# Kernel optimization log

Measured on AMD Instinct MI355X. Metric: run time of the kernel, lower is better.

The kernel has to match this reference:

```python
import jax, jax.numpy as jnp
import numpy as np

WS = 7
NUM_HEADS = 4


def setup_inputs() -> dict:
    key = jax.random.key(0)
    ks = jax.random.split(key, 5)
    C = 128
    return {
        "x": jax.random.normal(ks[0], (8, 222, 222, C), dtype=jnp.float32),
        "qkv_w": jax.random.normal(ks[1], (C, 3 * C), dtype=jnp.float32) * 0.02,
        "qkv_b": jax.random.normal(ks[2], (3 * C,), dtype=jnp.float32) * 0.02,
        "proj_w": jax.random.normal(ks[3], (C, C), dtype=jnp.float32) * 0.02,
        "proj_b": jax.random.normal(ks[4], (C,), dtype=jnp.float32) * 0.02,
    }


def reference(x, qkv_w, qkv_b, proj_w, proj_b):
    B, H, W, C = x.shape
    ws, nh = WS, NUM_HEADS
    hd = C // nh
    scale = hd ** (-0.5)
    pad_h = (ws - H % ws) % ws
    pad_w = (ws - W % ws) % ws
    xp = jnp.pad(x, ((0, 0), (0, pad_h), (0, pad_w), (0, 0)))
    Hp, Wp = H + pad_h, W + pad_w
    # window partition: [B,Hp,Wp,C] -> [nW, ws*ws, C]
    xw = xp.reshape(B, Hp // ws, ws, Wp // ws, ws, C)
    xw = xw.transpose(0, 1, 3, 2, 4, 5).reshape(-1, ws * ws, C)
    # qkv projection
    qkv = xw @ qkv_w + qkv_b  # [nW, 49, 3C]
    qkv = qkv.reshape(-1, ws * ws, 3, nh, hd).transpose(2, 0, 3, 1, 4)
    q, k, v = qkv[0], qkv[1], qkv[2]  # each [nW, nh, 49, hd]
    attn = jax.nn.softmax(jnp.einsum('whqd,whkd->whqk', q, k) * scale, axis=-1)
    out = jnp.einsum('whqk,whkd->whqd', attn, v)  # [nW, nh, 49, hd]
    out = out.transpose(0, 2, 1, 3).reshape(-1, ws * ws, C)
    out = out @ proj_w + proj_b
    # window reverse: [nW, ws*ws, C] -> [B, Hp, Wp, C]
    out = out.reshape(B, Hp // ws, Wp // ws, ws, ws, C)
    out = out.transpose(0, 1, 3, 2, 4, 5).reshape(B, Hp, Wp, C)
    return out[:, :H, :W, :]
```

## Files before the change

kernel.cpp:

```cpp
#include <hip/hip_runtime.h>
#include <stdint.h>

typedef __attribute__((ext_vector_type(8))) short bf16x8;
typedef __attribute__((ext_vector_type(4))) float f32x4;

#define IMG 222

__device__ __forceinline__ unsigned short f2bf(float f){
  unsigned int u = __float_as_uint(f);
  return (unsigned short)((u + 0x7fffu + ((u >> 16) & 1u)) >> 16);
}

__device__ __forceinline__ int sw128(int r, int c){ return r*128 + (c ^ ((r & 7) << 3)); }
__device__ __forceinline__ int sw64 (int r, int c){ return r*64  + (c ^ ((r & 7) << 3)); }

__global__ void prep_weights(const float* __restrict__ qkv_w,
                             const float* __restrict__ proj_w,
                             unsigned short* __restrict__ qwt,
                             unsigned short* __restrict__ pwt){
  int i = blockIdx.x * blockDim.x + threadIdx.x;
  if (i < 384*128){ int n = i >> 7, k = i & 127; qwt[i] = f2bf(qkv_w[k*384 + n]); }
  if (i < 128*128){ int n = i >> 7, k = i & 127; pwt[i] = f2bf(proj_w[k*128 + n]); }
}

__global__ __launch_bounds__(256, 3)
void win_attn(const float* __restrict__ x,
              const float* __restrict__ qkv_b,
              const float* __restrict__ proj_b,
              const unsigned short* __restrict__ qwt,
              const unsigned short* __restrict__ pwt,
              float* __restrict__ out)
{
  extern __shared__ unsigned short lds[];
  unsigned short* r0 = lds;
  unsigned short* r1 = lds + 8192;
  unsigned short* r2 = lds + 16384;

  const int tid = threadIdx.x;
  const int wid = tid >> 6;
  const int l   = tid & 63;
  const int l15 = l & 15;
  const int lhi = l >> 4;

  const int w  = blockIdx.x;
  const int b  = w >> 10;
  const int wi = (w >> 5) & 31;
  const int wj = w & 31;

  {
    const int t  = tid >> 2;
    const int cb = (tid & 3) * 32;
    const int r  = t / 7, c = t - r*7;
    const int gh = wi*7 + r, gw = wj*7 + c;
    const bool valid = (t < 49) && (gh < IMG) && (gw < IMG);
    const float* src = x + (((size_t)((size_t)b*IMG + gh))*IMG + gw)*128 + cb;
    #pragma unroll
    for (int i = 0; i < 8; ++i){
      float4 v = valid ? *(const float4*)(src + i*4) : make_float4(0.f,0.f,0.f,0.f);
      unsigned short* dst = r0 + sw128(t, cb + i*4);
      dst[0] = f2bf(v.x); dst[1] = f2bf(v.y); dst[2] = f2bf(v.z); dst[3] = f2bf(v.w);
    }
  }
  __syncthreads();

  bf16x8 a[4][4];
  #pragma unroll
  for (int mi = 0; mi < 4; ++mi)
    #pragma unroll
    for (int ks = 0; ks < 4; ++ks)
      a[mi][ks] = *(const bf16x8*)(r0 + sw128(mi*16 + l15, ks*32 + lhi*8));
  __syncthreads();

  const float scale = 0.17677669529663687f;

  #pragma unroll
  for (int nj = 0; nj < 6; ++nj){
    const int ni = wid + nj*4;
    bf16x8 bfr[4];
    #pragma unroll
    for (int ks = 0; ks < 4; ++ks)
      bfr[ks] = *(const bf16x8*)(qwt + (ni*16 + l15)*128 + ks*32 + lhi*8);
    const float bias = qkv_b[ni*16 + l15];
    #pragma unroll
    for (int mi = 0; mi < 4; ++mi){
      f32x4 acc = {0.f,0.f,0.f,0.f};
      #pragma unroll
      for (int ks = 0; ks < 4; ++ks)
        acc = __builtin_amdgcn_mfma_f32_16x16x32_bf16(a[mi][ks], bfr[ks], acc, 0, 0, 0);
      #pragma unroll
      for (int r = 0; r < 4; ++r){
        float val = acc[r] + bias;
        int row = mi*16 + lhi*4 + r;
        int col = ni*16 + l15;
        if (ni < 8){
          r0[sw128(row, col)] = f2bf(val * scale);
        } else if (ni < 16){
          r1[sw128(row, col - 128)] = f2bf(val);
        } else {
          r2[sw64(col - 256, row)] = f2bf(val);
        }
      }
    }
  }
  __syncthreads();

  const int h = wid;
  f32x4 sacc[4][4];
  {
    bf16x8 aq[4], bk[4];
    #pragma unroll
    for (int i = 0; i < 4; ++i){
      aq[i] = *(const bf16x8*)(r0 + sw128(i*16 + l15, h*32 + lhi*8));
      bk[i] = *(const bf16x8*)(r1 + sw128(i*16 + l15, h*32 + lhi*8));
    }
    #pragma unroll
    for (int mi = 0; mi < 4; ++mi)
      #pragma unroll
      for (int ni = 0; ni < 4; ++ni){
        f32x4 z = {0.f,0.f,0.f,0.f};
        sacc[mi][ni] = __builtin_amdgcn_mfma_f32_16x16x32_bf16(aq[mi], bk[ni], z, 0, 0, 0);
      }
  }
  __syncthreads();

  unsigned short* pb = lds + h*4096;
  if (l15 > 0){
    #pragma unroll
    for (int mi = 0; mi < 4; ++mi)
      #pragma unroll
      for (int r = 0; r < 4; ++r)
        sacc[mi][3][r] = -1e30f;
  }
  #pragma unroll
  for (int mi = 0; mi < 4; ++mi){
    #pragma unroll
    for (int r = 0; r < 4; ++r){
      float m = fmaxf(fmaxf(sacc[mi][0][r], sacc[mi][1][r]),
                      fmaxf(sacc[mi][2][r], sacc[mi][3][r]));
      m = fmaxf(m, __shfl_xor(m, 1));
      m = fmaxf(m, __shfl_xor(m, 2));
      m = fmaxf(m, __shfl_xor(m, 4));
      m = fmaxf(m, __shfl_xor(m, 8));
      float e0 = __expf(sacc[mi][0][r] - m);
      float e1 = __expf(sacc[mi][1][r] - m);
      float e2 = __expf(sacc[mi][2][r] - m);
      float e3 = __expf(sacc[mi][3][r] - m);
      float s = e0 + e1 + e2 + e3;
      s += __shfl_xor(s, 1); s += __shfl_xor(s, 2);
      s += __shfl_xor(s, 4); s += __shfl_xor(s, 8);
      float inv = 1.0f / s;
      int row = mi*16 + lhi*4 + r;
      pb[sw64(row, l15)]      = f2bf(e0*inv);
      pb[sw64(row, l15 + 16)] = f2bf(e1*inv);
      pb[sw64(row, l15 + 32)] = f2bf(e2*inv);
      pb[sw64(row, l15 + 48)] = f2bf(e3*inv);
    }
  }

  bf16x8 pa[4][2], bv[2][2];
  #pragma unroll
  for (int mi = 0; mi < 4; ++mi)
    #pragma unroll
    for (int ks = 0; ks < 2; ++ks)
      pa[mi][ks] = *(const bf16x8*)(pb + sw64(mi*16 + l15, ks*32 + lhi*8));
  #pragma unroll
  for (int ni = 0; ni < 2; ++ni)
    #pragma unroll
    for (int ks = 0; ks < 2; ++ks)
      bv[ni][ks] = *(const bf16x8*)(r2 + sw64(h*32 + ni*16 + l15, ks*32 + lhi*8));
  __syncthreads();

  f32x4 oacc[4][2];
  #pragma unroll
  for (int mi = 0; mi < 4; ++mi)
    #pragma unroll
    for (int ni = 0; ni < 2; ++ni){
      f32x4 acc = {0.f,0.f,0.f,0.f};
      acc = __builtin_amdgcn_mfma_f32_16x16x32_bf16(pa[mi][0], bv[ni][0], acc, 0, 0, 0);
      acc = __builtin_amdgcn_mfma_f32_16x16x32_bf16(pa[mi][1], bv[ni][1], acc, 0, 0, 0);
      oacc[mi][ni] = acc;
    }
  #pragma unroll
  for (int mi = 0; mi < 4; ++mi)
    #pragma unroll
    for (int ni = 0; ni < 2; ++ni)
      #pragma unroll
      for (int r = 0; r < 4; ++r)
        r2[sw128(mi*16 + lhi*4 + r, h*32 + ni*16 + l15)] = f2bf(oacc[mi][ni][r]);
  __syncthreads();

  bf16x8 ao[4][4];
  #pragma unroll
  for (int mi = 0; mi < 4; ++mi)
    #pragma unroll
    for (int ks = 0; ks < 4; ++ks)
      ao[mi][ks] = *(const bf16x8*)(r2 + sw128(mi*16 + l15, ks*32 + lhi*8));

  #pragma unroll
  for (int nj = 0; nj < 2; ++nj){
    const int ni = wid + nj*4;
    bf16x8 pbw[4];
    #pragma unroll
    for (int ks = 0; ks < 4; ++ks)
      pbw[ks] = *(const bf16x8*)(pwt + (ni*16 + l15)*128 + ks*32 + lhi*8);
    const float bias = proj_b[ni*16 + l15];
    #pragma unroll
    for (int mi = 0; mi < 4; ++mi){
      f32x4 acc = {0.f,0.f,0.f,0.f};
      #pragma unroll
      for (int ks = 0; ks < 4; ++ks)
        acc = __builtin_amdgcn_mfma_f32_16x16x32_bf16(ao[mi][ks], pbw[ks], acc, 0, 0, 0);
      #pragma unroll
      for (int r = 0; r < 4; ++r){
        int t = mi*16 + lhi*4 + r;
        if (t < 49){
          int rr = t / 7, cc = t - rr*7;
          int gh = wi*7 + rr, gw = wj*7 + cc;
          if (gh < IMG && gw < IMG)
            out[(((size_t)((size_t)b*IMG + gh))*IMG + gw)*128 + ni*16 + l15] = acc[r] + bias;
        }
      }
    }
  }
}

extern "C" void kernel_launch(void* const* d_in, const int* in_sizes, int n_in,
                              void* d_out, int out_size, void* d_ws, size_t ws_size,
                              hipStream_t stream) {
  const float* x      = (const float*)d_in[0];
  const float* qkv_w  = (const float*)d_in[1];
  const float* qkv_b  = (const float*)d_in[2];
  const float* proj_w = (const float*)d_in[3];
  const float* proj_b = (const float*)d_in[4];
  float* out = (float*)d_out;

  unsigned short* qwt = (unsigned short*)d_ws;
  unsigned short* pwt = qwt + 384*128;

  hipLaunchKernelGGL(prep_weights, dim3(192), dim3(256), 0, stream,
                     qkv_w, proj_w, qwt, pwt);
  hipLaunchKernelGGL(win_attn, dim3(8192), dim3(256), 49152, stream,
                     x, qkv_b, proj_b, qwt, pwt, out);
}
```

Before: 256.1 us.

## Swap MFMA operand order for vectorized stores and defer softmax normalization

Swaps the A/B operands of the QKV, QK^T, PV and projection MFMAs so each lane holds four consecutive output columns. That lets LDS writes use ushort4 and the global output use float4 instead of scalar stores. Softmax now reduces across lane groups with two shuffles instead of four, and its 1/sum scaling is applied after the PV product. The block index is also remapped so consecutive blocks interleave batches, and the input-tile LDS store is vectorized. The main risk is subtle layout or masking errors from the transposed fragment ownership.

```diff
diff --git a/kernel.cpp b/kernel.cpp
--- a/kernel.cpp
+++ b/kernel.cpp
@@ -42,7 +42,7 @@
   const int l15 = l & 15;
   const int lhi = l >> 4;
 
-  const int w  = blockIdx.x;
+  const int w  = (blockIdx.x & 7) * 1024 + (blockIdx.x >> 3);
   const int b  = w >> 10;
   const int wi = (w >> 5) & 31;
   const int wj = w & 31;
@@ -57,8 +57,8 @@
     #pragma unroll
     for (int i = 0; i < 8; ++i){
       float4 v = valid ? *(const float4*)(src + i*4) : make_float4(0.f,0.f,0.f,0.f);
-      unsigned short* dst = r0 + sw128(t, cb + i*4);
-      dst[0] = f2bf(v.x); dst[1] = f2bf(v.y); dst[2] = f2bf(v.z); dst[3] = f2bf(v.w);
+      *(ushort4*)(r0 + sw128(t, cb + i*4)) =
+        make_ushort4(f2bf(v.x), f2bf(v.y), f2bf(v.z), f2bf(v.w));
     }
   }
   __syncthreads();
@@ -80,113 +80,111 @@
     #pragma unroll
     for (int ks = 0; ks < 4; ++ks)
       bfr[ks] = *(const bf16x8*)(qwt + (ni*16 + l15)*128 + ks*32 + lhi*8);
-    const float bias = qkv_b[ni*16 + l15];
-    #pragma unroll
-    for (int mi = 0; mi < 4; ++mi){
+    if (nj < 4){
+      const float4 bias4 = *(const float4*)(qkv_b + ni*16 + lhi*4);
+      #pragma unroll
+      for (int mi = 0; mi < 4; ++mi){
+        f32x4 acc = {0.f,0.f,0.f,0.f};
+        #pragma unroll
+        for (int ks = 0; ks < 4; ++ks)
+          acc = __builtin_amdgcn_mfma_f32_16x16x32_bf16(bfr[ks], a[mi][ks], acc, 0, 0, 0);
+        if (nj < 2){
+          *(ushort4*)(r0 + sw128(mi*16 + l15, ni*16 + lhi*4)) =
+            make_ushort4(f2bf((acc[0]+bias4.x)*scale), f2bf((acc[1]+bias4.y)*scale),
+                         f2bf((acc[2]+bias4.z)*scale), f2bf((acc[3]+bias4.w)*scale));
+        } else {
+          *(ushort4*)(r1 + sw128(mi*16 + l15, (ni-8)*16 + lhi*4)) =
+            make_ushort4(f2bf(acc[0]+bias4.x), f2bf(acc[1]+bias4.y),
+                         f2bf(acc[2]+bias4.z), f2bf(acc[3]+bias4.w));
+        }
+      }
+    } else {
+      const float bias = qkv_b[ni*16 + l15];
+      #pragma unroll
+      for (int mi = 0; mi < 4; ++mi){
+        f32x4 acc = {0.f,0.f,0.f,0.f};
+        #pragma unroll
+        for (int ks = 0; ks < 4; ++ks)
+          acc = __builtin_amdgcn_mfma_f32_16x16x32_bf16(a[mi][ks], bfr[ks], acc, 0, 0, 0);
+        *(ushort4*)(r2 + sw64((ni-16)*16 + l15, mi*16 + lhi*4)) =
+          make_ushort4(f2bf(acc[0]+bias), f2bf(acc[1]+bias),
+                       f2bf(acc[2]+bias), f2bf(acc[3]+bias));
+      }
+    }
+  }
+  __syncthreads();
+
+  const int h = wid;
+  unsigned short* ph = lds + h*4096;
+  bf16x8 aq[4], bk[4];
+  #pragma unroll
+  for (int i = 0; i < 4; ++i){
+    aq[i] = *(const bf16x8*)(r0 + sw128(i*16 + l15, h*32 + lhi*8));
+    bk[i] = *(const bf16x8*)(r1 + sw128(i*16 + l15, h*32 + lhi*8));
+  }
+  __syncthreads();
+
+  float invs[4];
+  #pragma unroll
+  for (int mi = 0; mi < 4; ++mi){
+    f32x4 st[4];
+    #pragma unroll
+    for (int ni = 0; ni < 4; ++ni){
+      f32x4 z = {0.f,0.f,0.f,0.f};
+      st[ni] = __builtin_amdgcn_mfma_f32_16x16x32_bf16(bk[ni], aq[mi], z, 0, 0, 0);
+    }
+    st[3][1] = -1e30f; st[3][2] = -1e30f; st[3][3] = -1e30f;
+    if (lhi != 0) st[3][0] = -1e30f;
+    float m = st[0][0];
+    #pragma unroll
+    for (int ni = 0; ni < 4; ++ni)
+      #pragma unroll
+      for (int r = 0; r < 4; ++r)
+        m = fmaxf(m, st[ni][r]);
+    m = fmaxf(m, __shfl_xor(m, 16));
+    m = fmaxf(m, __shfl_xor(m, 32));
+    float e[4][4], s = 0.f;
+    #pragma unroll
+    for (int ni = 0; ni < 4; ++ni)
+      #pragma unroll
+      for (int r = 0; r < 4; ++r){
+        e[ni][r] = __expf(st[ni][r] - m);
+        s += e[ni][r];
+      }
+    s += __shfl_xor(s, 16);
+    s += __shfl_xor(s, 32);
+    invs[mi] = __builtin_amdgcn_rcpf(s);
+    #pragma unroll
+    for (int ni = 0; ni < 4; ++ni)
+      *(ushort4*)(ph + sw64(mi*16 + l15, ni*16 + lhi*4)) =
+        make_ushort4(f2bf(e[ni][0]), f2bf(e[ni][1]), f2bf(e[ni][2]), f2bf(e[ni][3]));
+  }
+
+  bf16x8 pa[4][2], bv[2][2];
+  #pragma unroll
+  for (int mi = 0; mi < 4; ++mi)
+    #pragma unroll
+    for (int ks = 0; ks < 2; ++ks)
+      pa[mi][ks] = *(const bf16x8*)(ph + sw64(mi*16 + l15, ks*32 + lhi*8));
+  #pragma unroll
+  for (int nc = 0; nc < 2; ++nc)
+    #pragma unroll
+    for (int ks = 0; ks < 2; ++ks)
+      bv[nc][ks] = *(const bf16x8*)(r2 + sw64(h*32 + nc*16 + l15, ks*32 + lhi*8));
+  __syncthreads();
+
+  #pragma unroll
+  for (int mi = 0; mi < 4; ++mi){
+    const float is = invs[mi];
+    #pragma unroll
+    for (int nc = 0; nc < 2; ++nc){
       f32x4 acc = {0.f,0.f,0.f,0.f};
-      #pragma unroll
-      for (int ks = 0; ks < 4; ++ks)
-        acc = __builtin_amdgcn_mfma_f32_16x16x32_bf16(a[mi][ks], bfr[ks], acc, 0, 0, 0);
-      #pragma unroll
-      for (int r = 0; r < 4; ++r){
-        float val = acc[r] + bias;
-        int row = mi*16 + lhi*4 + r;
-        int col = ni*16 + l15;
-        if (ni < 8){
-          r0[sw128(row, col)] = f2bf(val * scale);
-        } else if (ni < 16){
-          r1[sw128(row, col - 128)] = f2bf(val);
-        } else {
-          r2[sw64(col - 256, row)] = f2bf(val);
-        }
-      }
-    }
-  }
-  __syncthreads();
-
-  const int h = wid;
-  f32x4 sacc[4][4];
-  {
-    bf16x8 aq[4], bk[4];
-    #pragma unroll
-    for (int i = 0; i < 4; ++i){
-      aq[i] = *(const bf16x8*)(r0 + sw128(i*16 + l15, h*32 + lhi*8));
-      bk[i] = *(const bf16x8*)(r1 + sw128(i*16 + l15, h*32 + lhi*8));
-    }
-    #pragma unroll
-    for (int mi = 0; mi < 4; ++mi)
-      #pragma unroll
-      for (int ni = 0; ni < 4; ++ni){
-        f32x4 z = {0.f,0.f,0.f,0.f};
-        sacc[mi][ni] = __builtin_amdgcn_mfma_f32_16x16x32_bf16(aq[mi], bk[ni], z, 0, 0, 0);
-      }
-  }
-  __syncthreads();
-
-  unsigned short* pb = lds + h*4096;
-  if (l15 > 0){
-    #pragma unroll
-    for (int mi = 0; mi < 4; ++mi)
-      #pragma unroll
-      for (int r = 0; r < 4; ++r)
-        sacc[mi][3][r] = -1e30f;
-  }
-  #pragma unroll
-  for (int mi = 0; mi < 4; ++mi){
-    #pragma unroll
-    for (int r = 0; r < 4; ++r){
-      float m = fmaxf(fmaxf(sacc[mi][0][r], sacc[mi][1][r]),
-                      fmaxf(sacc[mi][2][r], sacc[mi][3][r]));
-      m = fmaxf(m, __shfl_xor(m, 1));
-      m = fmaxf(m, __shfl_xor(m, 2));
-      m = fmaxf(m, __shfl_xor(m, 4));
-      m = fmaxf(m, __shfl_xor(m, 8));
-      float e0 = __expf(sacc[mi][0][r] - m);
-      float e1 = __expf(sacc[mi][1][r] - m);
-      float e2 = __expf(sacc[mi][2][r] - m);
-      float e3 = __expf(sacc[mi][3][r] - m);
-      float s = e0 + e1 + e2 + e3;
-      s += __shfl_xor(s, 1); s += __shfl_xor(s, 2);
-      s += __shfl_xor(s, 4); s += __shfl_xor(s, 8);
-      float inv = 1.0f / s;
-      int row = mi*16 + lhi*4 + r;
-      pb[sw64(row, l15)]      = f2bf(e0*inv);
-      pb[sw64(row, l15 + 16)] = f2bf(e1*inv);
-      pb[sw64(row, l15 + 32)] = f2bf(e2*inv);
-      pb[sw64(row, l15 + 48)] = f2bf(e3*inv);
-    }
-  }
-
-  bf16x8 pa[4][2], bv[2][2];
-  #pragma unroll
-  for (int mi = 0; mi < 4; ++mi)
-    #pragma unroll
-    for (int ks = 0; ks < 2; ++ks)
-      pa[mi][ks] = *(const bf16x8*)(pb + sw64(mi*16 + l15, ks*32 + lhi*8));
-  #pragma unroll
-  for (int ni = 0; ni < 2; ++ni)
-    #pragma unroll
-    for (int ks = 0; ks < 2; ++ks)
-      bv[ni][ks] = *(const bf16x8*)(r2 + sw64(h*32 + ni*16 + l15, ks*32 + lhi*8));
-  __syncthreads();
-
-  f32x4 oacc[4][2];
-  #pragma unroll
-  for (int mi = 0; mi < 4; ++mi)
-    #pragma unroll
-    for (int ni = 0; ni < 2; ++ni){
-      f32x4 acc = {0.f,0.f,0.f,0.f};
-      acc = __builtin_amdgcn_mfma_f32_16x16x32_bf16(pa[mi][0], bv[ni][0], acc, 0, 0, 0);
-      acc = __builtin_amdgcn_mfma_f32_16x16x32_bf16(pa[mi][1], bv[ni][1], acc, 0, 0, 0);
-      oacc[mi][ni] = acc;
-    }
-  #pragma unroll
-  for (int mi = 0; mi < 4; ++mi)
-    #pragma unroll
-    for (int ni = 0; ni < 2; ++ni)
-      #pragma unroll
-      for (int r = 0; r < 4; ++r)
-        r2[sw128(mi*16 + lhi*4 + r, h*32 + ni*16 + l15)] = f2bf(oacc[mi][ni][r]);
+      acc = __builtin_amdgcn_mfma_f32_16x16x32_bf16(bv[nc][0], pa[mi][0], acc, 0, 0, 0);
+      acc = __builtin_amdgcn_mfma_f32_16x16x32_bf16(bv[nc][1], pa[mi][1], acc, 0, 0, 0);
+      *(ushort4*)(r2 + sw128(mi*16 + l15, h*32 + nc*16 + lhi*4)) =
+        make_ushort4(f2bf(acc[0]*is), f2bf(acc[1]*is), f2bf(acc[2]*is), f2bf(acc[3]*is));
+    }
+  }
   __syncthreads();
 
   bf16x8 ao[4][4];
@@ -203,21 +201,21 @@
     #pragma unroll
     for (int ks = 0; ks < 4; ++ks)
       pbw[ks] = *(const bf16x8*)(pwt + (ni*16 + l15)*128 + ks*32 + lhi*8);
-    const float bias = proj_b[ni*16 + l15];
+    const float4 bias4 = *(const float4*)(proj_b + ni*16 + lhi*4);
     #pragma unroll
     for (int mi = 0; mi < 4; ++mi){
       f32x4 acc = {0.f,0.f,0.f,0.f};
       #pragma unroll
       for (int ks = 0; ks < 4; ++ks)
-        acc = __builtin_amdgcn_mfma_f32_16x16x32_bf16(ao[mi][ks], pbw[ks], acc, 0, 0, 0);
-      #pragma unroll
-      for (int r = 0; r < 4; ++r){
-        int t = mi*16 + lhi*4 + r;
-        if (t < 49){
-          int rr = t / 7, cc = t - rr*7;
-          int gh = wi*7 + rr, gw = wj*7 + cc;
-          if (gh < IMG && gw < IMG)
-            out[(((size_t)((size_t)b*IMG + gh))*IMG + gw)*128 + ni*16 + l15] = acc[r] + bias;
+        acc = __builtin_amdgcn_mfma_f32_16x16x32_bf16(pbw[ks], ao[mi][ks], acc, 0, 0, 0);
+      const int t = mi*16 + l15;
+      if (t < 49){
+        const int rr = t / 7, cc = t - rr*7;
+        const int gh = wi*7 + rr, gw = wj*7 + cc;
+        if (gh < IMG && gw < IMG){
+          float4 o = make_float4(acc[0]+bias4.x, acc[1]+bias4.y,
+                                 acc[2]+bias4.z, acc[3]+bias4.w);
+          *(float4*)(out + (((size_t)((size_t)b*IMG + gh))*IMG + gw)*128 + ni*16 + lhi*4) = o;
         }
       }
     }
```

New measurement: 215.3 us. 1.19x faster.
